# Optimization experiments

Measured on AMD Instinct MI355X. Metric: run time of the kernel, lower is better.

## Reference

```python
import jax, jax.numpy as jnp
import numpy as np

B, S, D, H, BLEN, FF = 4, 4096, 1024, 16, 256, 4096
DH = D // H
NEG = -1e9
EPS = 1e-6


def setup_inputs() -> dict:
    key = jax.random.key(0)
    ks = jax.random.split(key, 8)
    s = 0.02
    return {
        "X": jax.random.normal(ks[0], (B, S, D), jnp.float32),
        "Wq": jax.random.normal(ks[1], (D, D), jnp.float32) * s,
        "Wk": jax.random.normal(ks[2], (D, D), jnp.float32) * s,
        "Wv": jax.random.normal(ks[3], (D, D), jnp.float32) * s,
        "Wo": jax.random.normal(ks[4], (D, D), jnp.float32) * s,
        "g_attn": jnp.ones((D,), jnp.float32),
        "b_attn": jnp.zeros((D,), jnp.float32),
        "W1": jax.random.normal(ks[5], (D, FF), jnp.float32) * s,
        "b1": jnp.zeros((FF,), jnp.float32),
        "W2": jax.random.normal(ks[6], (FF, D), jnp.float32) * s,
        "b2": jnp.zeros((D,), jnp.float32),
        "g_ffn": jnp.ones((D,), jnp.float32),
        "b_ffn": jnp.zeros((D,), jnp.float32),
    }


def _layernorm(x, g, b):
    mu = jnp.mean(x, axis=-1, keepdims=True)
    var = jnp.mean(jnp.square(x - mu), axis=-1, keepdims=True)
    return (x - mu) * jax.lax.rsqrt(var + EPS) * g + b


def _local_attn(X, Wq, Wk, Wv, Wo):
    def split_heads(y):  # [B,S,D] -> [B,H,S,DH]
        return y.reshape(B, S, H, DH).transpose(0, 2, 1, 3)

    q = split_heads(X @ Wq) * (DH ** -0.5)
    k = split_heads(X @ Wk)
    v = split_heads(X @ Wv)

    nb = S // BLEN  # S is a multiple of BLEN, so the torch pad is a no-op
    q = q.reshape(B, H, nb, BLEN, DH)
    k = k.reshape(B, H, nb, BLEN, DH)
    v = v.reshape(B, H, nb, BLEN, DH)

    # First block: plain causal attention within block 0.
    causal = NEG * jnp.triu(jnp.ones((BLEN, BLEN), jnp.float32), 1)
    logits0 = jnp.einsum('bhkd,bhqd->bhqk', k[:, :, 0], q[:, :, 0]) + causal
    out0 = jax.nn.softmax(logits0, axis=-1) @ v[:, :, 0]  # [B,H,BLEN,DH]

    # Tail blocks attend to [previous block, current block].
    local_k = jnp.concatenate([k[:, :, :-1], k[:, :, 1:]], axis=3)  # [B,H,nb-1,2B,DH]
    local_v = jnp.concatenate([v[:, :, :-1], v[:, :, 1:]], axis=3)
    tail_q = q[:, :, 1:]
    bias = NEG * jnp.triu(jnp.ones((BLEN, 2 * BLEN), jnp.float32), BLEN + 1)
    logits = jnp.einsum('bhnkd,bhnqd->bhnqk', local_k, tail_q) + bias
    tail = jnp.einsum('bhnqk,bhnkd->bhnqd', jax.nn.softmax(logits, axis=-1), local_v)
    tail = tail.reshape(B, H, S - BLEN, DH)

    res = jnp.concatenate([out0, tail], axis=2)       # [B,H,S,DH]
    res = res.transpose(0, 2, 1, 3).reshape(B, S, D)  # merge heads
    return res @ Wo


def reference(X, Wq, Wk, Wv, Wo, g_attn, b_attn, W1, b1, W2, b2, g_ffn, b_ffn):
    y = _local_attn(X, Wq, Wk, Wv, Wo)
    X = _layernorm(y + X, g_attn, b_attn)
    y = jax.nn.relu(X @ W1 + b1) @ W2 + b2
    X = _layernorm(y + X, g_ffn, b_ffn)
    return X
```

## Files before the change

kernel.cpp:

```cpp
#include <hip/hip_runtime.h>
#include <stdint.h>

#define B_    4
#define S_    4096
#define D_    1024
#define H_    16
#define DH_   64
#define BLEN_ 256
#define FF_   4096
#define M_    16384

typedef unsigned short u16;
typedef __attribute__((ext_vector_type(8))) short s8v;
typedef __attribute__((ext_vector_type(4))) short s4v;
typedef __attribute__((ext_vector_type(4))) float f4v;

#define MFMA32(A,B,C) __builtin_amdgcn_mfma_f32_16x16x32_bf16(A,B,C,0,0,0)
#define BAR() asm volatile("s_barrier" ::: "memory")
#define SCHEDB() __builtin_amdgcn_sched_barrier(0)

__device__ __forceinline__ f4v mfma16(s4v a, s4v b, f4v c) {
#if defined(__HIP_DEVICE_COMPILE__)
#if __has_builtin(__builtin_amdgcn_mfma_f32_16x16x16bf16_1k)
  return __builtin_amdgcn_mfma_f32_16x16x16bf16_1k(a, b, c, 0, 0, 0);
#elif __has_builtin(__builtin_amdgcn_mfma_f32_16x16x16_bf16_1k)
  return __builtin_amdgcn_mfma_f32_16x16x16_bf16_1k(a, b, c, 0, 0, 0);
#elif __has_builtin(__builtin_amdgcn_mfma_f32_16x16x16_bf16)
  return __builtin_amdgcn_mfma_f32_16x16x16_bf16(a, b, c, 0, 0, 0);
#else
  f4v d;
  asm volatile("v_mfma_f32_16x16x16_bf16 %0, %1, %2, %3"
               : "=v"(d) : "v"(a), "v"(b), "v"(c));
  return d;
#endif
#else
  (void)a; (void)b; return c;
#endif
}

__device__ __forceinline__ u16 f2b(float f) {
  union { float f; unsigned u; } v; v.f = f;
  unsigned r = v.u + 0x7fffu + ((v.u >> 16) & 1u);
  return (u16)(r >> 16);
}
__device__ __forceinline__ float b2f(u16 h) {
  union { unsigned u; float f; } v; v.u = ((unsigned)h) << 16; return v.f;
}

__device__ __forceinline__ void gld16(const void* gp, void* lp) {
  __builtin_amdgcn_global_load_lds(
      (const __attribute__((address_space(1))) void*)(uintptr_t)gp,
      (__attribute__((address_space(3))) void*)(uintptr_t)lp, 16, 0, 0);
}


__global__ __launch_bounds__(256) void k_castx(const float* __restrict__ in, u16* __restrict__ out) {
  long i = (long)blockIdx.x * 256 + threadIdx.x;
  float4 v = ((const float4*)in)[i];
  s4v o; o[0] = (short)f2b(v.x); o[1] = (short)f2b(v.y);
  o[2] = (short)f2b(v.z); o[3] = (short)f2b(v.w);
  *(s4v*)(out + i * 4) = o;
}

__global__ __launch_bounds__(256) void k_wt(const float* __restrict__ in, u16* __restrict__ out,
                                            int K, int N, float scale) {
  __shared__ u16 tile[32][33];
  const int tx = threadIdx.x & 31, ty = threadIdx.x >> 5;
  const int kb = blockIdx.y << 5, nb = blockIdx.x << 5;
#pragma unroll
  for (int r = 0; r < 4; r++) {
    int row = ty + r * 8;
    tile[row][tx] = f2b(in[(long)(kb + row) * N + nb + tx] * scale);
  }
  __syncthreads();
#pragma unroll
  for (int r = 0; r < 4; r++) {
    int row = ty + r * 8;
    out[(long)(nb + row) * K + kb + tx] = tile[tx][row];
  }
}

template<int EPI, int K, int NB>
__global__ __launch_bounds__(512, 2) void k_gemm256(
    const u16* __restrict__ A, const u16* __restrict__ Bt,
    const float* __restrict__ bias, const void* __restrict__ res,
    u16* __restrict__ out, int N) {
  __shared__ __align__(16) u16 sA[2][16384];
  __shared__ __align__(16) u16 sB[2][16384];
  const int t = threadIdx.x, lane = t & 63, w = t >> 6;
  const int wm = w >> 2, wn = w & 3;
  const int nwg = gridDim.x, cpx = nwg >> 3, orig = blockIdx.x;
  const int wg = (orig & 7) * cpx + (orig >> 3);
  const int nb = wg % NB, mb = wg / NB;
  const int m0 = mb << 8, n0 = nb << 8;
  constexpr int NT = K >> 6;

  const int srow = lane >> 3;
  const int scol = ((lane & 7) ^ srow) << 3;
  const u16* gA = A + (size_t)(m0 + srow) * K + scol;
  const u16* gB = Bt + (size_t)(n0 + srow) * K + scol;

  auto stA = [&](int d, int h, int kt) {
#pragma unroll
    for (int i = 0; i < 2; i++) {
      int c = i * 8 + w;
      gld16(gA + (size_t)(h * 128 + c * 8) * K + kt * 64, &sA[d][h * 8192 + c * 512]);
    }
  };
  auto stB = [&](int d, int h, int kt) {
#pragma unroll
    for (int i = 0; i < 2; i++) {
      int c = i * 8 + w;
      gld16(gB + (size_t)(h * 128 + c * 8) * K + kt * 64, &sB[d][h * 8192 + c * 512]);
    }
  };

  const int swz = (lane & 7) << 4;
  const int g8b = (lane >> 4) << 4;
  const int r16 = lane & 15;
  auto rdA = [&](int d, int mt, int kh) -> s8v {
    int byt = (mt * 32 + wm * 16 + r16) * 128 + ((kh * 64 + g8b) ^ swz);
    return *(const s8v*)((const char*)sA[d] + byt);
  };
  auto rdB = [&](int d, int nt, int kh) -> s8v {
    int byt = (nt * 64 + wn * 16 + r16) * 128 + ((kh * 64 + g8b) ^ swz);
    return *(const s8v*)((const char*)sB[d] + byt);
  };

  f4v acc[8][4];
  f4v zz = {0.f, 0.f, 0.f, 0.f};
#pragma unroll
  for (int i = 0; i < 8; i++)
#pragma unroll
    for (int j = 0; j < 4; j++) acc[i][j] = zz;

  stA(0, 0, 0); stA(0, 1, 0); stB(0, 0, 0); stB(0, 1, 0);
  asm volatile("s_waitcnt vmcnt(0)" ::: "memory");
  BAR();

  s8v a0[4][2], a1[4][2], bb[4][2];
#pragma unroll
  for (int m = 0; m < 4; m++) { a0[m][0] = rdA(0, m, 0); a0[m][1] = rdA(0, m, 1); }
#pragma unroll
  for (int n = 0; n < 4; n++) { bb[n][0] = rdB(0, n, 0); bb[n][1] = rdB(0, n, 1); }
  SCHEDB();

  for (int j = 0; j < NT; ++j) {
    const int d = j & 1, nd = d ^ 1;
    const bool s1 = (j + 1 < NT);

    if (s1) { stA(nd, 0, j + 1); stA(nd, 1, j + 1); stB(nd, 0, j + 1); stB(nd, 1, j + 1); }
#pragma unroll
    for (int m = 0; m < 4; m++) { a1[m][0] = rdA(d, m + 4, 0); a1[m][1] = rdA(d, m + 4, 1); }
    SCHEDB();
    __builtin_amdgcn_s_setprio(1);
#pragma unroll
    for (int m = 0; m < 4; m++)
#pragma unroll
      for (int n = 0; n < 4; n++) {
        acc[m][n] = MFMA32(a0[m][0], bb[n][0], acc[m][n]);
        acc[m][n] = MFMA32(a0[m][1], bb[n][1], acc[m][n]);
      }
    __builtin_amdgcn_s_setprio(0);
    SCHEDB();
    asm volatile("s_waitcnt lgkmcnt(0)" ::: "memory");
    if (s1) asm volatile("s_waitcnt vmcnt(0)" ::: "memory");
    BAR();
    __builtin_amdgcn_s_setprio(1);
#pragma unroll
    for (int m = 0; m < 4; m++)
#pragma unroll
      for (int n = 0; n < 2; n++) {
        acc[m + 4][n] = MFMA32(a1[m][0], bb[n][0], acc[m + 4][n]);
        acc[m + 4][n] = MFMA32(a1[m][1], bb[n][1], acc[m + 4][n]);
      }
    __builtin_amdgcn_s_setprio(0);
    SCHEDB();
    if (s1) {
#pragma unroll
      for (int m = 0; m < 4; m++) { a0[m][0] = rdA(nd, m, 0); a0[m][1] = rdA(nd, m, 1); }
    }
    SCHEDB();
    __builtin_amdgcn_s_setprio(1);
#pragma unroll
    for (int m = 0; m < 4; m++)
#pragma unroll
      for (int n = 0; n < 2; n++) {
        acc[m + 4][n + 2] = MFMA32(a1[m][0], bb[n + 2][0], acc[m + 4][n + 2]);
        acc[m + 4][n + 2] = MFMA32(a1[m][1], bb[n + 2][1], acc[m + 4][n + 2]);
      }
    __builtin_amdgcn_s_setprio(0);
    SCHEDB();
    if (s1) {
#pragma unroll
      for (int n = 0; n < 4; n++) { bb[n][0] = rdB(nd, n, 0); bb[n][1] = rdB(nd, n, 1); }
    }
    SCHEDB();
  }

  const int g4 = (lane >> 4) << 2;
#pragma unroll
  for (int mt = 0; mt < 8; mt++) {
#pragma unroll
    for (int nt = 0; nt < 4; nt++) {
      const int col = n0 + nt * 64 + wn * 16 + r16;
      const long rbase = m0 + mt * 32 + wm * 16 + g4;
      float bcol = 0.f;
      if constexpr (EPI == 2 || EPI == 3) bcol = bias[col];
#pragma unroll
      for (int r = 0; r < 4; r++) {
        long idx = (rbase + r) * (long)N + col;
        float v = acc[mt][nt][r];
        if constexpr (EPI == 1) v += ((const float*)res)[idx];
        if constexpr (EPI == 2) { v += bcol; v = fmaxf(v, 0.f); }
        if constexpr (EPI == 3) { v += bcol + b2f(((const u16*)res)[idx]); }
        out[idx] = f2b(v);
      }
    }
  }
}

__global__ __launch_bounds__(256) void k_attn(const u16* __restrict__ QKV, u16* __restrict__ Aout) {
  __shared__ __align__(16) u16 sK[64 * 64];
  __shared__ __align__(16) u16 sVT[64 * 64];
  const int t = threadIdx.x, lane = t & 63, w = t >> 6;
  const int qblock = blockIdx.x;
  const int b = blockIdx.y >> 4, h = blockIdx.y & 15;
  const int qcol = lane & 15, g = lane >> 4, g4 = g << 2;
  const int win = (qblock == 0) ? 0 : (qblock - 1) * BLEN_;
  const int nch = (qblock == 0) ? 4 : 8;
  const int qbw = qblock * BLEN_ + w * 64;
  const long rowbase = (long)b * S_;
  const int LDQ = 3072;

  s8v qf[4][2];
#pragma unroll
  for (int nt = 0; nt < 4; nt++)
#pragma unroll
    for (int kh = 0; kh < 2; kh++)
      qf[nt][kh] = *(const s8v*)(QKV + (rowbase + qbw + nt * 16 + qcol) * LDQ + h * DH_ + kh * 32 + (g << 3));

  f4v zz = {0.f, 0.f, 0.f, 0.f};
  f4v acc[4][4];
#pragma unroll
  for (int i = 0; i < 4; i++)
#pragma unroll
    for (int j = 0; j < 4; j++) acc[i][j] = zz;
  float mrow[4] = {-1e30f, -1e30f, -1e30f, -1e30f};
  float lrow[4] = {0.f, 0.f, 0.f, 0.f};

  for (int c = 0; c < nch; ++c) {
    const int kb = win + c * 64;
    __syncthreads();
#pragma unroll
    for (int p = 0; p < 2; p++) {
      int key = p * 32 + (t >> 3);
      int d8 = (t & 7) << 3;
      s8v kv = *(const s8v*)(QKV + (rowbase + kb + key) * LDQ + 1024 + h * DH_ + d8);
      int bo = key * 128 + d8 * 2; bo ^= (key & 7) << 4;
      *(s8v*)((char*)sK + bo) = kv;
    }
#pragma unroll
    for (int p = 0; p < 2; p++) {
      int key = (t & 31) + (p << 5);
      int d8 = (t >> 5) << 3;
      s8v vv = *(const s8v*)(QKV + (rowbase + kb + key) * LDQ + 2048 + h * DH_ + d8);
#pragma unroll
      for (int j = 0; j < 8; j++) {
        int dh = d8 + j;
        int bo = dh * 128 + key * 2; bo ^= (dh & 7) << 3;
        *(u16*)((char*)sVT + bo) = (u16)vv[j];
      }
    }
    __syncthreads();
    if (kb > qbw + 63) continue;

    f4v st[4][4];
#pragma unroll
    for (int i = 0; i < 4; i++)
#pragma unroll
      for (int j = 0; j < 4; j++) st[i][j] = zz;
#pragma unroll
    for (int kh = 0; kh < 2; kh++) {
#pragma unroll
      for (int mt = 0; mt < 4; mt++) {
        int key = mt * 16 + qcol;
        int bo = key * 128 + kh * 64 + (g << 4); bo ^= (key & 7) << 4;
        s8v kf = *(const s8v*)((const char*)sK + bo);
#pragma unroll
        for (int nt = 0; nt < 4; nt++) st[mt][nt] = MFMA32(kf, qf[nt][kh], st[mt][nt]);
      }
    }
    if (kb + 63 > qbw) {
#pragma unroll
      for (int mt = 0; mt < 4; mt++) {
        int kbase = kb + mt * 16 + g4;
#pragma unroll
        for (int nt = 0; nt < 4; nt++) {
          int qabs = qbw + nt * 16 + qcol;
#pragma unroll
          for (int r = 0; r < 4; r++)
            if (kbase + r > qabs) st[mt][nt][r] = -1e30f;
        }
      }
    }
    s4v pf[4][4];
#pragma unroll
    for (int nt = 0; nt < 4; nt++) {
      float cm = -1e30f;
#pragma unroll
      for (int mt = 0; mt < 4; mt++)
#pragma unroll
        for (int r = 0; r < 4; r++) cm = fmaxf(cm, st[mt][nt][r]);
      cm = fmaxf(cm, __shfl_xor(cm, 16));
      cm = fmaxf(cm, __shfl_xor(cm, 32));
      float mnew = fmaxf(mrow[nt], cm);
      float sc = __expf(mrow[nt] - mnew);
      mrow[nt] = mnew;
      float ps = 0.f;
#pragma unroll
      for (int kt = 0; kt < 4; kt++) {
        s4v pp;
#pragma unroll
        for (int r = 0; r < 4; r++) {
          float sv = st[kt][nt][r];
          float p = (sv > -1e29f) ? __expf(sv - mnew) : 0.f;
          ps += p;
          pp[r] = (short)f2b(p);
        }
        pf[nt][kt] = pp;
      }
      ps += __shfl_xor(ps, 16);
      ps += __shfl_xor(ps, 32);
      lrow[nt] = lrow[nt] * sc + ps;
#pragma unroll
      for (int dt = 0; dt < 4; dt++) acc[dt][nt] *= sc;
    }
#pragma unroll
    for (int dt = 0; dt < 4; dt++) {
      int dh = dt * 16 + qcol;
#pragma unroll
      for (int kt = 0; kt < 4; kt++) {
        int bo = dh * 128 + kt * 32 + (g << 3); bo ^= (dh & 7) << 3;
        s4v vf = *(const s4v*)((const char*)sVT + bo);
#pragma unroll
        for (int nt = 0; nt < 4; nt++) acc[dt][nt] = mfma16(vf, pf[nt][kt], acc[dt][nt]);
      }
    }
  }

#pragma unroll
  for (int nt = 0; nt < 4; nt++) {
    float inv = 1.f / lrow[nt];
    long qrow = rowbase + qbw + nt * 16 + qcol;
#pragma unroll
    for (int dt = 0; dt < 4; dt++) {
      s4v o;
#pragma unroll
      for (int r = 0; r < 4; r++) o[r] = (short)f2b(acc[dt][nt][r] * inv);
      *(s4v*)(Aout + qrow * D_ + h * DH_ + dt * 16 + g4) = o;
    }
  }
}

template<int OUTB>
__global__ __launch_bounds__(256) void k_ln(const u16* __restrict__ in, const float* __restrict__ gw,
                                            const float* __restrict__ bw, float* __restrict__ outf,
                                            u16* __restrict__ outb) {
  const int t = threadIdx.x, lane = t & 63, w = t >> 6;
  const long base = (long)blockIdx.x * D_;
  s4v xv = *(const s4v*)(in + base + t * 4);
  float v0 = b2f((u16)xv[0]), v1 = b2f((u16)xv[1]), v2 = b2f((u16)xv[2]), v3 = b2f((u16)xv[3]);
  float s = v0 + v1 + v2 + v3;
  float s2 = v0 * v0 + v1 * v1 + v2 * v2 + v3 * v3;
#pragma unroll
  for (int off = 1; off < 64; off <<= 1) { s += __shfl_xor(s, off); s2 += __shfl_xor(s2, off); }
  __shared__ float red[8];
  if (lane == 0) { red[w] = s; red[4 + w] = s2; }
  __syncthreads();
  s = red[0] + red[1] + red[2] + red[3];
  s2 = red[4] + red[5] + red[6] + red[7];
  float mu = s * (1.f / D_);
  float var = s2 * (1.f / D_) - mu * mu;
  float rstd = rsqrtf(var + 1e-6f);
  float4 gv = ((const float4*)gw)[t];
  float4 bv = ((const float4*)bw)[t];
  float o0 = (v0 - mu) * rstd * gv.x + bv.x;
  float o1 = (v1 - mu) * rstd * gv.y + bv.y;
  float o2 = (v2 - mu) * rstd * gv.z + bv.z;
  float o3 = (v3 - mu) * rstd * gv.w + bv.w;
  if constexpr (OUTB) {
    s4v o; o[0] = (short)f2b(o0); o[1] = (short)f2b(o1); o[2] = (short)f2b(o2); o[3] = (short)f2b(o3);
    *(s4v*)(outb + base + t * 4) = o;
  } else {
    float4 o; o.x = o0; o.y = o1; o.z = o2; o.w = o3;
    *(float4*)(outf + base + t * 4) = o;
  }
}


extern "C" void kernel_launch(void* const* d_in, const int* in_sizes, int n_in,
                              void* d_out, int out_size, void* d_ws, size_t ws_size,
                              hipStream_t stream) {
  const float* X      = (const float*)d_in[0];
  const float* Wq     = (const float*)d_in[1];
  const float* Wk     = (const float*)d_in[2];
  const float* Wv     = (const float*)d_in[3];
  const float* Wo     = (const float*)d_in[4];
  const float* g_attn = (const float*)d_in[5];
  const float* b_attn = (const float*)d_in[6];
  const float* W1     = (const float*)d_in[7];
  const float* b1     = (const float*)d_in[8];
  const float* W2     = (const float*)d_in[9];
  const float* b2     = (const float*)d_in[10];
  const float* g_ffn  = (const float*)d_in[11];
  const float* b_ffn  = (const float*)d_in[12];
  float* out = (float*)d_out;

  char* ws = (char*)d_ws;
  const size_t MB = 1ull << 20;
  u16* WqkvT = (u16*)(ws + 0 * MB);
  u16* WoT   = (u16*)(ws + 6 * MB);
  u16* W1T   = (u16*)(ws + 8 * MB);
  u16* W2T   = (u16*)(ws + 16 * MB);
  u16* Xb    = (u16*)(ws + 24 * MB);
  u16* QKVb  = (u16*)(ws + 56 * MB);
  u16* Ab    = (u16*)(ws + 152 * MB);
  u16* Yb    = (u16*)(ws + 184 * MB);
  u16* Mid   = QKVb;

  dim3 b256(256), b512(512);
  k_wt<<<dim3(32, 32),  b256, 0, stream>>>(Wq, WqkvT,               1024, 1024, 0.125f);
  k_wt<<<dim3(32, 32),  b256, 0, stream>>>(Wk, WqkvT + 1024 * 1024, 1024, 1024, 1.0f);
  k_wt<<<dim3(32, 32),  b256, 0, stream>>>(Wv, WqkvT + 2048 * 1024, 1024, 1024, 1.0f);
  k_wt<<<dim3(32, 32),  b256, 0, stream>>>(Wo, WoT, 1024, 1024, 1.0f);
  k_wt<<<dim3(128, 32), b256, 0, stream>>>(W1, W1T, 1024, 4096, 1.0f);
  k_wt<<<dim3(32, 128), b256, 0, stream>>>(W2, W2T, 4096, 1024, 1.0f);
  k_castx<<<dim3(16384), b256, 0, stream>>>(X, Xb);

  k_gemm256<0, 1024, 12><<<dim3(768), b512, 0, stream>>>(Xb, WqkvT, nullptr, nullptr, QKVb, 3072);
  k_attn<<<dim3(16, B_ * H_), b256, 0, stream>>>(QKVb, Ab);
  k_gemm256<1, 1024, 4><<<dim3(256), b512, 0, stream>>>(Ab, WoT, nullptr, X, Yb, 1024);
  k_ln<1><<<dim3(16384), b256, 0, stream>>>(Yb, g_attn, b_attn, nullptr, Xb);
  k_gemm256<2, 1024, 16><<<dim3(1024), b512, 0, stream>>>(Xb, W1T, b1, nullptr, Mid, 4096);
  k_gemm256<3, 4096, 4><<<dim3(256), b512, 0, stream>>>(Mid, W2T, b2, Xb, Yb, 1024);
  k_ln<0><<<dim3(16384), b256, 0, stream>>>(Yb, g_ffn, b_ffn, out, nullptr);

  (void)in_sizes; (void)n_in; (void)out_size; (void)ws_size;
}
```

Measured before the change: 603.1 us.

## Switch GEMM to 32x32x16 MFMA and load B fragments directly from global

Rewrites the 256x256 GEMM main loop to use 32x32x16 bf16 MFMA with a 4x2 wave layout. Each wave now owns a 64x128 output tile. The B operand is no longer staged in shared memory; each lane reads its B fragments straight from global memory. This halves LDS use and removes the B LDS traffic. The cost is uncoalesced, latency-exposed global loads of B with no reuse across the waves that share the same columns.

```diff
diff --git a/kernel.cpp b/kernel.cpp
--- a/kernel.cpp
+++ b/kernel.cpp
@@ -14,11 +14,26 @@
 typedef __attribute__((ext_vector_type(8))) short s8v;
 typedef __attribute__((ext_vector_type(4))) short s4v;
 typedef __attribute__((ext_vector_type(4))) float f4v;
+typedef __attribute__((ext_vector_type(16))) float f16v;
 
 #define MFMA32(A,B,C) __builtin_amdgcn_mfma_f32_16x16x32_bf16(A,B,C,0,0,0)
 #define BAR() asm volatile("s_barrier" ::: "memory")
 #define SCHEDB() __builtin_amdgcn_sched_barrier(0)
 
+__device__ __forceinline__ f16v mfma3216(s8v a, s8v b, f16v c) {
+#if defined(__HIP_DEVICE_COMPILE__)
+#if __has_builtin(__builtin_amdgcn_mfma_f32_32x32x16_bf16)
+  return __builtin_amdgcn_mfma_f32_32x32x16_bf16(a, b, c, 0, 0, 0);
+#else
+  f16v d;
+  asm volatile("v_mfma_f32_32x32x16_bf16 %0, %1, %2, %3"
+               : "=v"(d) : "v"(a), "v"(b), "v"(c));
+  return d;
+#endif
+#else
+  (void)a; (void)b; return c;
+#endif
+}
 __device__ __forceinline__ f4v mfma16(s4v a, s4v b, f4v c) {
 #if defined(__HIP_DEVICE_COMPILE__)
 #if __has_builtin(__builtin_amdgcn_mfma_f32_16x16x16bf16_1k)
@@ -86,9 +101,8 @@
     const float* __restrict__ bias, const void* __restrict__ res,
     u16* __restrict__ out, int N) {
   __shared__ __align__(16) u16 sA[2][16384];
-  __shared__ __align__(16) u16 sB[2][16384];
   const int t = threadIdx.x, lane = t & 63, w = t >> 6;
-  const int wm = w >> 2, wn = w & 3;
+  const int wm = w >> 1, wn = w & 1;
   const int nwg = gridDim.x, cpx = nwg >> 3, orig = blockIdx.x;
   const int wg = (orig & 7) * cpx + (orig >> 3);
   const int nb = wg % NB, mb = wg / NB;
@@ -98,8 +112,6 @@
   const int srow = lane >> 3;
   const int scol = ((lane & 7) ^ srow) << 3;
   const u16* gA = A + (size_t)(m0 + srow) * K + scol;
-  const u16* gB = Bt + (size_t)(n0 + srow) * K + scol;
-
   auto stA = [&](int d, int h, int kt) {
 #pragma unroll
     for (int i = 0; i < 2; i++) {
@@ -107,110 +119,79 @@
       gld16(gA + (size_t)(h * 128 + c * 8) * K + kt * 64, &sA[d][h * 8192 + c * 512]);
     }
   };
-  auto stB = [&](int d, int h, int kt) {
-#pragma unroll
-    for (int i = 0; i < 2; i++) {
-      int c = i * 8 + w;
-      gld16(gB + (size_t)(h * 128 + c * 8) * K + kt * 64, &sB[d][h * 8192 + c * 512]);
-    }
-  };
-
-  const int swz = (lane & 7) << 4;
-  const int g8b = (lane >> 4) << 4;
-  const int r16 = lane & 15;
-  auto rdA = [&](int d, int mt, int kh) -> s8v {
-    int byt = (mt * 32 + wm * 16 + r16) * 128 + ((kh * 64 + g8b) ^ swz);
+
+  const int arow = wm * 64 + (lane & 31);
+  const int ag = (lane >> 5) << 4;
+  auto rdA32 = [&](int d, int mt, int ks) -> s8v {
+    int row = arow + mt * 32;
+    int byt = row * 128 + ((ks * 32 + ag) ^ ((row & 7) << 4));
     return *(const s8v*)((const char*)sA[d] + byt);
   };
-  auto rdB = [&](int d, int nt, int kh) -> s8v {
-    int byt = (nt * 64 + wn * 16 + r16) * 128 + ((kh * 64 + g8b) ^ swz);
-    return *(const s8v*)((const char*)sB[d] + byt);
+
+  const u16* gB = Bt + (size_t)(n0 + wn * 128 + (lane & 31)) * K + ((lane >> 5) << 3);
+  auto ldB = [&](int kt, int ks, int nt) -> s8v {
+    return *(const s8v*)(gB + (size_t)(nt * 32) * K + kt * 64 + ks * 16);
   };
 
-  f4v acc[8][4];
-  f4v zz = {0.f, 0.f, 0.f, 0.f};
+  f16v acc[8];
 #pragma unroll
   for (int i = 0; i < 8; i++)
 #pragma unroll
-    for (int j = 0; j < 4; j++) acc[i][j] = zz;
-
-  stA(0, 0, 0); stA(0, 1, 0); stB(0, 0, 0); stB(0, 1, 0);
+    for (int r = 0; r < 16; r++) acc[i][r] = 0.f;
+
+  stA(0, 0, 0); stA(0, 1, 0);
   asm volatile("s_waitcnt vmcnt(0)" ::: "memory");
   BAR();
 
-  s8v a0[4][2], a1[4][2], bb[4][2];
-#pragma unroll
-  for (int m = 0; m < 4; m++) { a0[m][0] = rdA(0, m, 0); a0[m][1] = rdA(0, m, 1); }
-#pragma unroll
-  for (int n = 0; n < 4; n++) { bb[n][0] = rdB(0, n, 0); bb[n][1] = rdB(0, n, 1); }
-  SCHEDB();
+  s8v aA[2][2], bB[2][4];
+  aA[0][0] = rdA32(0, 0, 0); aA[0][1] = rdA32(0, 1, 0);
+#pragma unroll
+  for (int nt = 0; nt < 4; nt++) bB[0][nt] = ldB(0, 0, nt);
 
   for (int j = 0; j < NT; ++j) {
     const int d = j & 1, nd = d ^ 1;
     const bool s1 = (j + 1 < NT);
-
-    if (s1) { stA(nd, 0, j + 1); stA(nd, 1, j + 1); stB(nd, 0, j + 1); stB(nd, 1, j + 1); }
-#pragma unroll
-    for (int m = 0; m < 4; m++) { a1[m][0] = rdA(d, m + 4, 0); a1[m][1] = rdA(d, m + 4, 1); }
-    SCHEDB();
-    __builtin_amdgcn_s_setprio(1);
-#pragma unroll
-    for (int m = 0; m < 4; m++)
-#pragma unroll
-      for (int n = 0; n < 4; n++) {
-        acc[m][n] = MFMA32(a0[m][0], bb[n][0], acc[m][n]);
-        acc[m][n] = MFMA32(a0[m][1], bb[n][1], acc[m][n]);
-      }
-    __builtin_amdgcn_s_setprio(0);
-    SCHEDB();
-    asm volatile("s_waitcnt lgkmcnt(0)" ::: "memory");
+    if (s1) { stA(nd, 0, j + 1); stA(nd, 1, j + 1); }
+#pragma unroll
+    for (int ks = 0; ks < 4; ks++) {
+      const int cur = ks & 1, nxt = cur ^ 1;
+      if (ks < 3) {
+        aA[nxt][0] = rdA32(d, 0, ks + 1); aA[nxt][1] = rdA32(d, 1, ks + 1);
+#pragma unroll
+        for (int nt = 0; nt < 4; nt++) bB[nxt][nt] = ldB(j, ks + 1, nt);
+      } else if (s1) {
+#pragma unroll
+        for (int nt = 0; nt < 4; nt++) bB[nxt][nt] = ldB(j + 1, 0, nt);
+      }
+      SCHEDB();
+      __builtin_amdgcn_s_setprio(1);
+#pragma unroll
+      for (int mt = 0; mt < 2; mt++)
+#pragma unroll
+        for (int nt = 0; nt < 4; nt++)
+          acc[mt * 4 + nt] = mfma3216(aA[cur][mt], bB[cur][nt], acc[mt * 4 + nt]);
+      __builtin_amdgcn_s_setprio(0);
+      SCHEDB();
+    }
     if (s1) asm volatile("s_waitcnt vmcnt(0)" ::: "memory");
     BAR();
-    __builtin_amdgcn_s_setprio(1);
-#pragma unroll
-    for (int m = 0; m < 4; m++)
-#pragma unroll
-      for (int n = 0; n < 2; n++) {
-        acc[m + 4][n] = MFMA32(a1[m][0], bb[n][0], acc[m + 4][n]);
-        acc[m + 4][n] = MFMA32(a1[m][1], bb[n][1], acc[m + 4][n]);
-      }
-    __builtin_amdgcn_s_setprio(0);
-    SCHEDB();
-    if (s1) {
-#pragma unroll
-      for (int m = 0; m < 4; m++) { a0[m][0] = rdA(nd, m, 0); a0[m][1] = rdA(nd, m, 1); }
-    }
-    SCHEDB();
-    __builtin_amdgcn_s_setprio(1);
-#pragma unroll
-    for (int m = 0; m < 4; m++)
-#pragma unroll
-      for (int n = 0; n < 2; n++) {
-        acc[m + 4][n + 2] = MFMA32(a1[m][0], bb[n + 2][0], acc[m + 4][n + 2]);
-        acc[m + 4][n + 2] = MFMA32(a1[m][1], bb[n + 2][1], acc[m + 4][n + 2]);
-      }
-    __builtin_amdgcn_s_setprio(0);
-    SCHEDB();
-    if (s1) {
-#pragma unroll
-      for (int n = 0; n < 4; n++) { bb[n][0] = rdB(nd, n, 0); bb[n][1] = rdB(nd, n, 1); }
-    }
-    SCHEDB();
-  }
-
-  const int g4 = (lane >> 4) << 2;
-#pragma unroll
-  for (int mt = 0; mt < 8; mt++) {
+    if (s1) { aA[0][0] = rdA32(nd, 0, 0); aA[0][1] = rdA32(nd, 1, 0); }
+  }
+
+  const int r4 = (lane >> 5) << 2;
+#pragma unroll
+  for (int mt = 0; mt < 2; mt++) {
 #pragma unroll
     for (int nt = 0; nt < 4; nt++) {
-      const int col = n0 + nt * 64 + wn * 16 + r16;
-      const long rbase = m0 + mt * 32 + wm * 16 + g4;
+      const int col = n0 + wn * 128 + nt * 32 + (lane & 31);
+      const long rbase = m0 + wm * 64 + mt * 32 + r4;
       float bcol = 0.f;
       if constexpr (EPI == 2 || EPI == 3) bcol = bias[col];
 #pragma unroll
-      for (int r = 0; r < 4; r++) {
-        long idx = (rbase + r) * (long)N + col;
-        float v = acc[mt][nt][r];
+      for (int reg = 0; reg < 16; reg++) {
+        long row = rbase + (reg & 3) + 8 * (reg >> 2);
+        long idx = row * (long)N + col;
+        float v = acc[mt * 4 + nt][reg];
         if constexpr (EPI == 1) v += ((const float*)res)[idx];
         if constexpr (EPI == 2) { v += bcol; v = fmaxf(v, 0.f); }
         if constexpr (EPI == 3) { v += bcol + b2f(((const u16*)res)[idx]); }
```

New measurement: 1.080 ms. 1.79x slower.

## Replace 256x256 GEMM tiles with simpler 128x128 four-wave kernel

Applied to the files above, without the earlier changes.

Replaces the 512-thread 256x256 tile GEMM, with its hand-scheduled split register prefetch and sched barriers, by a 256-thread 128x128 tile kernel. The new kernel reads all A/B fragments from LDS each k-step and issues its MFMAs in one block. Grids grow fourfold, which should improve load balance and occupancy across CUs. In exchange it gives up the intra-iteration overlap of LDS reads with MFMAs and halves data reuse per tile, so global/LDS traffic per flop increases.

```diff
diff --git a/kernel.cpp b/kernel.cpp
--- a/kernel.cpp
+++ b/kernel.cpp
@@ -17,7 +17,6 @@
 
 #define MFMA32(A,B,C) __builtin_amdgcn_mfma_f32_16x16x32_bf16(A,B,C,0,0,0)
 #define BAR() asm volatile("s_barrier" ::: "memory")
-#define SCHEDB() __builtin_amdgcn_sched_barrier(0)
 
 __device__ __forceinline__ f4v mfma16(s4v a, s4v b, f4v c) {
 #if defined(__HIP_DEVICE_COMPILE__)
@@ -81,37 +80,36 @@
 }
 
 template<int EPI, int K, int NB>
-__global__ __launch_bounds__(512, 2) void k_gemm256(
+__global__ __launch_bounds__(256, 2) void k_gemm128(
     const u16* __restrict__ A, const u16* __restrict__ Bt,
     const float* __restrict__ bias, const void* __restrict__ res,
     u16* __restrict__ out, int N) {
-  __shared__ __align__(16) u16 sA[2][16384];
-  __shared__ __align__(16) u16 sB[2][16384];
+  __shared__ __align__(16) u16 sA[2][8192];
+  __shared__ __align__(16) u16 sB[2][8192];
   const int t = threadIdx.x, lane = t & 63, w = t >> 6;
-  const int wm = w >> 2, wn = w & 3;
+  const int wm = w >> 1, wn = w & 1;
   const int nwg = gridDim.x, cpx = nwg >> 3, orig = blockIdx.x;
   const int wg = (orig & 7) * cpx + (orig >> 3);
   const int nb = wg % NB, mb = wg / NB;
-  const int m0 = mb << 8, n0 = nb << 8;
+  const int m0 = mb << 7, n0 = nb << 7;
   constexpr int NT = K >> 6;
 
   const int srow = lane >> 3;
   const int scol = ((lane & 7) ^ srow) << 3;
   const u16* gA = A + (size_t)(m0 + srow) * K + scol;
   const u16* gB = Bt + (size_t)(n0 + srow) * K + scol;
-
-  auto stA = [&](int d, int h, int kt) {
-#pragma unroll
-    for (int i = 0; i < 2; i++) {
-      int c = i * 8 + w;
-      gld16(gA + (size_t)(h * 128 + c * 8) * K + kt * 64, &sA[d][h * 8192 + c * 512]);
+  auto stA = [&](int d, int kt) {
+#pragma unroll
+    for (int i = 0; i < 4; i++) {
+      int c = i * 4 + w;
+      gld16(gA + (size_t)(c * 8) * K + kt * 64, &sA[d][c * 512]);
     }
   };
-  auto stB = [&](int d, int h, int kt) {
-#pragma unroll
-    for (int i = 0; i < 2; i++) {
-      int c = i * 8 + w;
-      gld16(gB + (size_t)(h * 128 + c * 8) * K + kt * 64, &sB[d][h * 8192 + c * 512]);
+  auto stB = [&](int d, int kt) {
+#pragma unroll
+    for (int i = 0; i < 4; i++) {
+      int c = i * 4 + w;
+      gld16(gB + (size_t)(c * 8) * K + kt * 64, &sB[d][c * 512]);
     }
   };
 
@@ -119,92 +117,55 @@
   const int g8b = (lane >> 4) << 4;
   const int r16 = lane & 15;
   auto rdA = [&](int d, int mt, int kh) -> s8v {
-    int byt = (mt * 32 + wm * 16 + r16) * 128 + ((kh * 64 + g8b) ^ swz);
+    int byt = (wm * 64 + mt * 16 + r16) * 128 + ((kh * 64 + g8b) ^ swz);
     return *(const s8v*)((const char*)sA[d] + byt);
   };
   auto rdB = [&](int d, int nt, int kh) -> s8v {
-    int byt = (nt * 64 + wn * 16 + r16) * 128 + ((kh * 64 + g8b) ^ swz);
+    int byt = (wn * 64 + nt * 16 + r16) * 128 + ((kh * 64 + g8b) ^ swz);
     return *(const s8v*)((const char*)sB[d] + byt);
   };
 
-  f4v acc[8][4];
+  f4v acc[4][4];
   f4v zz = {0.f, 0.f, 0.f, 0.f};
 #pragma unroll
-  for (int i = 0; i < 8; i++)
+  for (int i = 0; i < 4; i++)
 #pragma unroll
     for (int j = 0; j < 4; j++) acc[i][j] = zz;
 
-  stA(0, 0, 0); stA(0, 1, 0); stB(0, 0, 0); stB(0, 1, 0);
+  stA(0, 0); stB(0, 0);
   asm volatile("s_waitcnt vmcnt(0)" ::: "memory");
   BAR();
-
-  s8v a0[4][2], a1[4][2], bb[4][2];
-#pragma unroll
-  for (int m = 0; m < 4; m++) { a0[m][0] = rdA(0, m, 0); a0[m][1] = rdA(0, m, 1); }
-#pragma unroll
-  for (int n = 0; n < 4; n++) { bb[n][0] = rdB(0, n, 0); bb[n][1] = rdB(0, n, 1); }
-  SCHEDB();
 
   for (int j = 0; j < NT; ++j) {
     const int d = j & 1, nd = d ^ 1;
     const bool s1 = (j + 1 < NT);
-
-    if (s1) { stA(nd, 0, j + 1); stA(nd, 1, j + 1); stB(nd, 0, j + 1); stB(nd, 1, j + 1); }
-#pragma unroll
-    for (int m = 0; m < 4; m++) { a1[m][0] = rdA(d, m + 4, 0); a1[m][1] = rdA(d, m + 4, 1); }
-    SCHEDB();
+    if (s1) { stA(nd, j + 1); stB(nd, j + 1); }
+    s8v av[4][2], bv[4][2];
+#pragma unroll
+    for (int mt = 0; mt < 4; mt++) { av[mt][0] = rdA(d, mt, 0); av[mt][1] = rdA(d, mt, 1); }
+#pragma unroll
+    for (int nt = 0; nt < 4; nt++) { bv[nt][0] = rdB(d, nt, 0); bv[nt][1] = rdB(d, nt, 1); }
     __builtin_amdgcn_s_setprio(1);
 #pragma unroll
-    for (int m = 0; m < 4; m++)
-#pragma unroll
-      for (int n = 0; n < 4; n++) {
-        acc[m][n] = MFMA32(a0[m][0], bb[n][0], acc[m][n]);
-        acc[m][n] = MFMA32(a0[m][1], bb[n][1], acc[m][n]);
+    for (int mt = 0; mt < 4; mt++)
+#pragma unroll
+      for (int nt = 0; nt < 4; nt++) {
+        acc[mt][nt] = MFMA32(av[mt][0], bv[nt][0], acc[mt][nt]);
+        acc[mt][nt] = MFMA32(av[mt][1], bv[nt][1], acc[mt][nt]);
       }
     __builtin_amdgcn_s_setprio(0);
-    SCHEDB();
     asm volatile("s_waitcnt lgkmcnt(0)" ::: "memory");
     if (s1) asm volatile("s_waitcnt vmcnt(0)" ::: "memory");
     BAR();
-    __builtin_amdgcn_s_setprio(1);
-#pragma unroll
-    for (int m = 0; m < 4; m++)
-#pragma unroll
-      for (int n = 0; n < 2; n++) {
-        acc[m + 4][n] = MFMA32(a1[m][0], bb[n][0], acc[m + 4][n]);
-        acc[m + 4][n] = MFMA32(a1[m][1], bb[n][1], acc[m + 4][n]);
-      }
-    __builtin_amdgcn_s_setprio(0);
-    SCHEDB();
-    if (s1) {
-#pragma unroll
-      for (int m = 0; m < 4; m++) { a0[m][0] = rdA(nd, m, 0); a0[m][1] = rdA(nd, m, 1); }
-    }
-    SCHEDB();
-    __builtin_amdgcn_s_setprio(1);
-#pragma unroll
-    for (int m = 0; m < 4; m++)
-#pragma unroll
-      for (int n = 0; n < 2; n++) {
-        acc[m + 4][n + 2] = MFMA32(a1[m][0], bb[n + 2][0], acc[m + 4][n + 2]);
-        acc[m + 4][n + 2] = MFMA32(a1[m][1], bb[n + 2][1], acc[m + 4][n + 2]);
-      }
-    __builtin_amdgcn_s_setprio(0);
-    SCHEDB();
-    if (s1) {
-#pragma unroll
-      for (int n = 0; n < 4; n++) { bb[n][0] = rdB(nd, n, 0); bb[n][1] = rdB(nd, n, 1); }
-    }
-    SCHEDB();
   }
 
   const int g4 = (lane >> 4) << 2;
 #pragma unroll
-  for (int mt = 0; mt < 8; mt++) {
+  for (int mt = 0; mt < 4; mt++) {
 #pragma unroll
     for (int nt = 0; nt < 4; nt++) {
-      const int col = n0 + nt * 64 + wn * 16 + r16;
-      const long rbase = m0 + mt * 32 + wm * 16 + g4;
+      const int col = n0 + wn * 64 + nt * 16 + r16;
+      const long rbase = m0 + wm * 64 + mt * 16 + g4;
       float bcol = 0.f;
       if constexpr (EPI == 2 || EPI == 3) bcol = bias[col];
 #pragma unroll
@@ -429,7 +390,7 @@
   u16* Yb    = (u16*)(ws + 184 * MB);
   u16* Mid   = QKVb;
 
-  dim3 b256(256), b512(512);
+  dim3 b256(256);
   k_wt<<<dim3(32, 32),  b256, 0, stream>>>(Wq, WqkvT,               1024, 1024, 0.125f);
   k_wt<<<dim3(32, 32),  b256, 0, stream>>>(Wk, WqkvT + 1024 * 1024, 1024, 1024, 1.0f);
   k_wt<<<dim3(32, 32),  b256, 0, stream>>>(Wv, WqkvT + 2048 * 1024, 1024, 1024, 1.0f);
@@ -438,12 +399,12 @@
   k_wt<<<dim3(32, 128), b256, 0, stream>>>(W2, W2T, 4096, 1024, 1.0f);
   k_castx<<<dim3(16384), b256, 0, stream>>>(X, Xb);
 
-  k_gemm256<0, 1024, 12><<<dim3(768), b512, 0, stream>>>(Xb, WqkvT, nullptr, nullptr, QKVb, 3072);
+  k_gemm128<0, 1024, 24><<<dim3(3072), b256, 0, stream>>>(Xb, WqkvT, nullptr, nullptr, QKVb, 3072);
   k_attn<<<dim3(16, B_ * H_), b256, 0, stream>>>(QKVb, Ab);
-  k_gemm256<1, 1024, 4><<<dim3(256), b512, 0, stream>>>(Ab, WoT, nullptr, X, Yb, 1024);
+  k_gemm128<1, 1024, 8><<<dim3(1024), b256, 0, stream>>>(Ab, WoT, nullptr, X, Yb, 1024);
   k_ln<1><<<dim3(16384), b256, 0, stream>>>(Yb, g_attn, b_attn, nullptr, Xb);
-  k_gemm256<2, 1024, 16><<<dim3(1024), b512, 0, stream>>>(Xb, W1T, b1, nullptr, Mid, 4096);
-  k_gemm256<3, 4096, 4><<<dim3(256), b512, 0, stream>>>(Mid, W2T, b2, Xb, Yb, 1024);
+  k_gemm128<2, 1024, 32><<<dim3(4096), b256, 0, stream>>>(Xb, W1T, b1, nullptr, Mid, 4096);
+  k_gemm128<3, 4096, 8><<<dim3(1024), b256, 0, stream>>>(Mid, W2T, b2, Xb, Yb, 1024);
   k_ln<0><<<dim3(16384), b256, 0, stream>>>(Yb, g_ffn, b_ffn, out, nullptr);
 
   (void)in_sizes; (void)n_in; (void)out_size; (void)ws_size;
```

Measured after the change: 637.7 us. +5.7%, slower.
